# Kernel tuning notes

Hardware: AMD Instinct MI355X
Metric: run time of the kernel (lower is better)

Reference implementation:

```python
import jax, jax.numpy as jnp
import numpy as np

N, E = 100000, 1600000
ENT, OCU, SAI, IJ = 64, 64, 64, 8


def setup_inputs() -> dict:
    key = jax.random.key(0)
    ks = jax.random.split(key, 14)

    def lin(k, fan_in, fan_out):
        s = 1.0 / np.sqrt(fan_in)
        kw, kb = jax.random.split(k)
        w = jax.random.uniform(kw, (fan_in, fan_out), minval=-s, maxval=s, dtype=jnp.float32)
        b = jax.random.uniform(kb, (fan_out,), minval=-s, maxval=s, dtype=jnp.float32)
        return w, b

    we_w1, we_b1 = lin(ks[0], 2 * ENT + 1 + IJ, OCU)
    we_w2, we_b2 = lin(ks[1], OCU, OCU)
    wx_w1, wx_b1 = lin(ks[2], OCU, OCU)
    wx_w2, wx_b2 = lin(ks[3], OCU, 1)
    wh_w1, wh_b1 = lin(ks[4], ENT + OCU, OCU)
    wh_w2, wh_b2 = lin(ks[5], OCU, SAI)
    wv_w1, wv_b1 = lin(ks[6], ENT, OCU)
    wv_w2, wv_b2 = lin(ks[7], OCU, 1)

    return {
        "h": jax.random.normal(ks[8], (N, ENT), dtype=jnp.float32),
        "x": jax.random.normal(ks[9], (N, 3), dtype=jnp.float32),
        "velocidade": jax.random.normal(ks[10], (N, 3), dtype=jnp.float32),
        "atributos_arestas": jax.random.normal(ks[11], (E, IJ), dtype=jnp.float32),
        "we_w1": we_w1, "we_b1": we_b1, "we_w2": we_w2, "we_b2": we_b2,
        "wx_w1": wx_w1, "wx_b1": wx_b1, "wx_w2": wx_w2, "wx_b2": wx_b2,
        "wh_w1": wh_w1, "wh_b1": wh_b1, "wh_w2": wh_w2, "wh_b2": wh_b2,
        "wv_w1": wv_w1, "wv_b1": wv_b1, "wv_w2": wv_w2, "wv_b2": wv_b2,
        "arestas": jax.random.randint(ks[12], (2, E), 0, N, dtype=jnp.int32),
    }


def reference(h, x, velocidade, atributos_arestas,
              we_w1, we_b1, we_w2, we_b2,
              wx_w1, wx_b1, wx_w2, wx_b2,
              wh_w1, wh_b1, wh_w2, wh_b2,
              wv_w1, wv_b1, wv_w2, wv_b2,
              arestas):
    linhas, cols = arestas[0], arestas[1]
    n = h.shape[0]

    # gather endpoint coordinates, radial distance per edge
    diferenca = x[linhas] - x[cols]                            # [E, 3]
    dif_radial = jnp.sum(diferenca * diferenca, axis=1, keepdims=True)  # [E, 1]

    # edge MLP phi_e on [h_i, h_j, ||x_i-x_j||^2, edge_attr]
    atributos = jnp.concatenate([h[linhas], h[cols], dif_radial, atributos_arestas], axis=1)
    m_ij = jnp.tanh(jnp.tanh(atributos @ we_w1 + we_b1) @ we_w2 + we_b2)   # [E, OCU]

    # phi_x: per-edge scalar gate on coordinate differences
    phi_x = jnp.tanh(jnp.tanh(m_ij @ wx_w1 + wx_b1) @ wx_w2 + wx_b2)       # [E, 1]

    # phi_v: per-node scalar gate on velocity
    phi_v = jnp.tanh(h @ wv_w1 + wv_b1) @ wv_w2 + wv_b2                    # [N, 1]

    # segment-mean of (diferenca * phi_x) over source nodes
    trans = diferenca * phi_x                                              # [E, 3]
    agg_sum = jax.ops.segment_sum(trans, linhas, num_segments=n)           # [N, 3]
    cnt = jax.ops.segment_sum(jnp.ones((E, 1), trans.dtype), linhas, num_segments=n)
    agg_mean = agg_sum / jnp.maximum(cnt, 1.0)

    velocidade_nova = velocidade * phi_v + agg_mean
    x_nova = x + velocidade_nova

    # segment-sum of edge messages, node update phi_h
    m_i = jax.ops.segment_sum(m_ij, linhas, num_segments=n)                # [N, OCU]
    h_cat = jnp.concatenate([h, m_i], axis=1)
    h_nova = jnp.tanh(h_cat @ wh_w1 + wh_b1) @ wh_w2 + wh_b2               # [N, SAI]

    return (h_nova, x_nova, velocidade_nova)
```

## Files before the change

### kernel.cpp

```cpp
#include <hip/hip_runtime.h>


typedef unsigned int uint;
typedef unsigned short u16;
typedef __attribute__((ext_vector_type(8))) short short8;
typedef __attribute__((ext_vector_type(4))) float f32x4;

#define UB_LO(u) __uint_as_float((u) << 16)
#define UB_HI(u) __uint_as_float((u) & 0xffff0000u)

__device__ __forceinline__ float fast_tanh(float x) {
    float e = __expf(2.0f * x);
    return 1.0f - 2.0f * __builtin_amdgcn_rcpf(e + 1.0f);
}
__device__ __forceinline__ u16 bf16rne(float f) {
    uint u = __float_as_uint(f);
    return (u16)((u + 0x7fffu + ((u >> 16) & 1u)) >> 16);
}
__device__ __forceinline__ uint packbf(float a, float b) {
    return (uint)bf16rne(a) | ((uint)bf16rne(b) << 16);
}
__device__ __forceinline__ uint packbf_fast(float a, float b) {
    return __builtin_amdgcn_perm(__float_as_uint(b), __float_as_uint(a), 0x07060302u);
}
__device__ __forceinline__ u16 trunc16(float f) {
    return (u16)(__float_as_uint(f) >> 16);
}
__device__ __forceinline__ int swzb(int b) { return b ^ ((b >> 3) & 0x70); }

__global__ void wprep_kernel(const float* __restrict__ we_w1, const float* __restrict__ we_w2,
                             const float* __restrict__ wx_w1, const float* __restrict__ wv_w1,
                             const float* __restrict__ wh_w1, const float* __restrict__ wh_w2,
                             u16* __restrict__ we1t, u16* __restrict__ we2t,
                             u16* __restrict__ wx1t, u16* __restrict__ wv1t,
                             u16* __restrict__ wh1t, u16* __restrict__ wh2t,
                             u16* __restrict__ wert) {
    int t = blockIdx.x * 256 + threadIdx.x;
    if (t < 8192) {
        int j = t >> 7, k = t & 127;
        we1t[t] = bf16rne(we_w1[k * 64 + j]);
        wh1t[t] = bf16rne(wh_w1[k * 64 + j]);
    }
    if (t < 4096) {
        int n = t >> 6, k = t & 63;
        we2t[t] = bf16rne(we_w2[k * 64 + n]);
        wx1t[t] = bf16rne(wx_w1[k * 64 + n]);
        wv1t[t] = bf16rne(wv_w1[k * 64 + n]);
        wh2t[t] = bf16rne(wh_w2[k * 64 + n]);
    }
    if (t < 2048) {
        int n = t >> 5, k = t & 31;
        float v = 0.0f;
        if (k == 0) v = we_w1[128 * 64 + n];
        else if (k <= 8) v = we_w1[(128 + k) * 64 + n];
        wert[t] = bf16rne(v);
    }
}

__global__ __launch_bounds__(256, 4)
void pre_mfma_kernel(const float* __restrict__ h, const float* __restrict__ we_b1,
                     const u16* __restrict__ we1t,
                     u16* __restrict__ HrB, u16* __restrict__ HcB, int N)
{
    __shared__ u16 X1[4096];
    __shared__ u16 X2[4096];
    const int tid = threadIdx.x, lane = tid & 63, wv = tid >> 6;
    const int nb = blockIdx.x * 64;
    const int el = tid >> 2, jg = tid & 3;
    const int fn = lane & 15, fk8 = (lane >> 4) * 8;

    {
        uint pk[8];
        if (nb + el < N) {
            const float4* h4 = (const float4*)(h + (size_t)(nb + el) * 64 + jg * 16);
            #pragma unroll
            for (int q = 0; q < 4; q++) {
                float4 v = h4[q];
                pk[2*q]   = packbf_fast(v.x, v.y);
                pk[2*q+1] = packbf_fast(v.z, v.w);
            }
        } else {
            #pragma unroll
            for (int q = 0; q < 8; q++) pk[q] = 0;
        }
        const int b0 = swzb(el * 128 + jg * 32), b1 = swzb(el * 128 + jg * 32 + 16);
        *(uint4*)(&X1[b0 >> 1]) = make_uint4(pk[0], pk[1], pk[2], pk[3]);
        *(uint4*)(&X1[b1 >> 1]) = make_uint4(pk[4], pk[5], pk[6], pk[7]);
    }
    __syncthreads();

    const int mb = wv * 16;
    short8 a0, a1;
    {
        const int ba = swzb((mb + fn) * 128 + fk8 * 2);
        const int bb = swzb((mb + fn) * 128 + 64 + fk8 * 2);
        a0 = *(const short8*)(&X1[ba >> 1]);
        a1 = *(const short8*)(&X1[bb >> 1]);
    }
    #pragma unroll
    for (int n0 = 0; n0 < 4; n0++) {
        uint4 bw0 = *(const uint4*)(we1t + (n0*16 + fn) * 128 + fk8);
        uint4 bw1 = *(const uint4*)(we1t + (n0*16 + fn) * 128 + 32 + fk8);
        const float bias = we_b1[n0 * 16 + fn];
        f32x4 q = {bias, bias, bias, bias};
        q = __builtin_amdgcn_mfma_f32_16x16x32_bf16(a0, __builtin_bit_cast(short8, bw0), q, 0, 0, 0);
        q = __builtin_amdgcn_mfma_f32_16x16x32_bf16(a1, __builtin_bit_cast(short8, bw1), q, 0, 0, 0);
        #pragma unroll
        for (int r2 = 0; r2 < 4; r2++) {
            const int m = mb + (lane >> 4) * 4 + r2;
            X2[swzb(m * 128 + (n0*16 + fn) * 2) >> 1] = bf16rne(q[r2]);
        }
    }
    __syncthreads();
    if (nb + el < N) {
        const int b0 = swzb(el * 128 + jg * 32), b1 = swzb(el * 128 + jg * 32 + 16);
        uint4 v0 = *(const uint4*)(&X2[b0 >> 1]);
        uint4 v1 = *(const uint4*)(&X2[b1 >> 1]);
        u16* o = HrB + (size_t)(nb + el) * 64 + jg * 16;
        *(uint4*)o = v0; *(uint4*)(o + 8) = v1;
    }
    __syncthreads();
    #pragma unroll
    for (int n0 = 0; n0 < 4; n0++) {
        uint4 bw0 = *(const uint4*)(we1t + (n0*16 + fn) * 128 + 64 + fk8);
        uint4 bw1 = *(const uint4*)(we1t + (n0*16 + fn) * 128 + 96 + fk8);
        f32x4 q = {0.f, 0.f, 0.f, 0.f};
        q = __builtin_amdgcn_mfma_f32_16x16x32_bf16(a0, __builtin_bit_cast(short8, bw0), q, 0, 0, 0);
        q = __builtin_amdgcn_mfma_f32_16x16x32_bf16(a1, __builtin_bit_cast(short8, bw1), q, 0, 0, 0);
        #pragma unroll
        for (int r2 = 0; r2 < 4; r2++) {
            const int m = mb + (lane >> 4) * 4 + r2;
            X2[swzb(m * 128 + (n0*16 + fn) * 2) >> 1] = bf16rne(q[r2]);
        }
    }
    __syncthreads();
    if (nb + el < N) {
        const int b0 = swzb(el * 128 + jg * 32), b1 = swzb(el * 128 + jg * 32 + 16);
        uint4 v0 = *(const uint4*)(&X2[b0 >> 1]);
        uint4 v1 = *(const uint4*)(&X2[b1 >> 1]);
        u16* o = HcB + (size_t)(nb + el) * 64 + jg * 16;
        *(uint4*)o = v0; *(uint4*)(o + 8) = v1;
    }
}

__global__ __launch_bounds__(256, 8)
void edge_mfma_kernel(const float* __restrict__ x, const float* __restrict__ eattr,
                      const int* __restrict__ perm, const int2* __restrict__ rc,
                      const u16* __restrict__ HrB, const u16* __restrict__ HcB,
                      const u16* __restrict__ wert,
                      const u16* __restrict__ we2t, const float* __restrict__ we_b2,
                      const u16* __restrict__ wx1t, const float* __restrict__ wx_b1,
                      const float* __restrict__ wx_w2, const float* __restrict__ wx_b2,
                      float* __restrict__ miF, float* __restrict__ aggF,
                      float* __restrict__ cntF, int E)
{
    __shared__ u16 T[4096];
    __shared__ float dS[64][3];
    __shared__ float pxS[64];
    __shared__ float radS[64];
    __shared__ int rS[64];

    const int tid = threadIdx.x, lane = tid & 63, wv = tid >> 6;
    int bid = blockIdx.x;
    const int nwg = gridDim.x;
    if ((nwg & 7) == 0) bid = (bid & 7) * (nwg >> 3) + (bid >> 3);
    const int sb = bid * 64;
    const int fn = lane & 15, fk8 = (lane >> 4) * 8;
    const int el = tid >> 2, jg = tid & 3;
    const int s = sb + el;
    const int mb = wv * 16;

    {
        int r = -1, c = 0;
        if (s < E) { int2 p2 = rc[s]; r = p2.x; c = p2.y; }
        if (jg == 0) rS[el] = r;
        uint pk[8];
        if (s < E) {
            if (jg == 0) {
                const float d0 = x[(size_t)r*3+0] - x[(size_t)c*3+0];
                const float d1 = x[(size_t)r*3+1] - x[(size_t)c*3+1];
                const float d2 = x[(size_t)r*3+2] - x[(size_t)c*3+2];
                dS[el][0] = d0; dS[el][1] = d1; dS[el][2] = d2;
                radS[el] = d0*d0 + d1*d1 + d2*d2;
            }
            uint4 ra = *(const uint4*)(HrB + (size_t)r * 64 + jg * 16);
            uint4 rb = *(const uint4*)(HrB + (size_t)r * 64 + jg * 16 + 8);
            uint4 ca = *(const uint4*)(HcB + (size_t)c * 64 + jg * 16);
            uint4 cb = *(const uint4*)(HcB + (size_t)c * 64 + jg * 16 + 8);
            uint rw[8] = {ra.x, ra.y, ra.z, ra.w, rb.x, rb.y, rb.z, rb.w};
            uint cw[8] = {ca.x, ca.y, ca.z, ca.w, cb.x, cb.y, cb.z, cb.w};
            #pragma unroll
            for (int q = 0; q < 8; q++) {
                const float lo = UB_LO(rw[q]) + UB_LO(cw[q]);
                const float hi = UB_HI(rw[q]) + UB_HI(cw[q]);
                pk[q] = packbf_fast(lo, hi);
            }
        } else {
            #pragma unroll
            for (int q = 0; q < 8; q++) pk[q] = 0;
        }
        const int b0 = swzb(el * 128 + jg * 32), b1 = swzb(el * 128 + jg * 32 + 16);
        *(uint4*)(&T[b0 >> 1]) = make_uint4(pk[0], pk[1], pk[2], pk[3]);
        *(uint4*)(&T[b1 >> 1]) = make_uint4(pk[4], pk[5], pk[6], pk[7]);
    }
    __syncthreads();

    uint ae[4] = {0, 0, 0, 0};
    {
        const int kc = lane >> 4;
        const int s2 = sb + mb + fn;
        if (kc < 2 && s2 < E) {
            const int e2 = perm[s2];
            const float4* ea4 = (const float4*)(eattr + (size_t)e2 * 8);
            if (kc == 0) {
                float4 u0 = ea4[0], u1 = ea4[1];
                const float rad = radS[mb + fn];
                ae[0] = packbf_fast(rad,  u0.x);
                ae[1] = packbf_fast(u0.y, u0.z);
                ae[2] = packbf_fast(u0.w, u1.x);
                ae[3] = packbf_fast(u1.y, u1.z);
            } else {
                float4 u1 = ea4[1];
                ae[0] = packbf_fast(u1.w, 0.0f);
            }
        }
    }
    const short8 a_e = __builtin_bit_cast(short8, *(uint4*)ae);

    #pragma unroll
    for (int n0 = 0; n0 < 4; n0++) {
        uint4 bw = *(const uint4*)(wert + (n0*16 + fn) * 32 + fk8);
        f32x4 q = {0.f, 0.f, 0.f, 0.f};
        q = __builtin_amdgcn_mfma_f32_16x16x32_bf16(a_e, __builtin_bit_cast(short8, bw), q, 0, 0, 0);
        #pragma unroll
        for (int r2 = 0; r2 < 4; r2++) {
            const int idx = swzb((mb + (lane >> 4) * 4 + r2) * 128 + (n0*16 + fn) * 2) >> 1;
            const float pre = q[r2] + UB_LO((uint)T[idx]);
            T[idx] = trunc16(fast_tanh(pre));
        }
    }

    short8 a0, a1;
    {
        const int ba = swzb((mb + fn) * 128 + fk8 * 2);
        const int bb = swzb((mb + fn) * 128 + 64 + fk8 * 2);
        a0 = *(const short8*)(&T[ba >> 1]);
        a1 = *(const short8*)(&T[bb >> 1]);
    }
    #pragma unroll
    for (int n0 = 0; n0 < 4; n0++) {
        uint4 bw0 = *(const uint4*)(we2t + (n0*16 + fn) * 64 + fk8);
        uint4 bw1 = *(const uint4*)(we2t + (n0*16 + fn) * 64 + 32 + fk8);
        const float bias = we_b2[n0 * 16 + fn];
        f32x4 q = {bias, bias, bias, bias};
        q = __builtin_amdgcn_mfma_f32_16x16x32_bf16(a0, __builtin_bit_cast(short8, bw0), q, 0, 0, 0);
        q = __builtin_amdgcn_mfma_f32_16x16x32_bf16(a1, __builtin_bit_cast(short8, bw1), q, 0, 0, 0);
        #pragma unroll
        for (int r2 = 0; r2 < 4; r2++) {
            const int m = mb + (lane >> 4) * 4 + r2;
            T[swzb(m * 128 + (n0*16 + fn) * 2) >> 1] = bf16rne(fast_tanh(q[r2]));
        }
    }

    short8 c0, c1;
    {
        const int ba = swzb((mb + fn) * 128 + fk8 * 2);
        const int bb = swzb((mb + fn) * 128 + 64 + fk8 * 2);
        c0 = *(const short8*)(&T[ba >> 1]);
        c1 = *(const short8*)(&T[bb >> 1]);
    }
    float pxp[4] = {0.f, 0.f, 0.f, 0.f};
    #pragma unroll
    for (int n0 = 0; n0 < 4; n0++) {
        uint4 bw0 = *(const uint4*)(wx1t + (n0*16 + fn) * 64 + fk8);
        uint4 bw1 = *(const uint4*)(wx1t + (n0*16 + fn) * 64 + 32 + fk8);
        const float bias = wx_b1[n0 * 16 + fn];
        f32x4 q = {bias, bias, bias, bias};
        q = __builtin_amdgcn_mfma_f32_16x16x32_bf16(c0, __builtin_bit_cast(short8, bw0), q, 0, 0, 0);
        q = __builtin_amdgcn_mfma_f32_16x16x32_bf16(c1, __builtin_bit_cast(short8, bw1), q, 0, 0, 0);
        const float wqn = wx_w2[n0 * 16 + fn];
        #pragma unroll
        for (int r2 = 0; r2 < 4; r2++) pxp[r2] += fast_tanh(q[r2]) * wqn;
    }
    #pragma unroll
    for (int off = 1; off < 16; off <<= 1) {
        #pragma unroll
        for (int r2 = 0; r2 < 4; r2++) pxp[r2] += __shfl_xor(pxp[r2], off, 64);
    }
    if (fn == 0) {
        const float bx2 = wx_b2[0];
        #pragma unroll
        for (int r2 = 0; r2 < 4; r2++) {
            const int m = mb + (lane >> 4) * 4 + r2;
            pxS[m] = fast_tanh(pxp[r2] + bx2);
        }
    }
    __syncthreads();

    const int w16 = wv * 16;
    for (int s0 = w16; s0 < w16 + 16; s0++) {
        const int r0 = rS[s0];
        if (r0 < 0) continue;
        if (s0 > 0 && rS[s0 - 1] == r0) continue;
        int s1 = s0 + 1;
        while (s1 < 64 && rS[s1] == r0) s1++;
        float msum = 0.0f, tsum = 0.0f;
        for (int t = s0; t < s1; t++) {
            msum += UB_LO((uint)T[swzb(t * 128 + lane * 2) >> 1]);
            if (lane < 3) tsum += dS[t][lane] * pxS[t];
        }
        atomicAdd(&miF[(size_t)r0 * 64 + lane], msum);
        if (lane < 3) atomicAdd(&aggF[(size_t)r0 * 3 + lane], tsum);
        if (lane == 3) atomicAdd(&cntF[r0], (float)(s1 - s0));
    }
}

__global__ __launch_bounds__(256, 4)
void aggnode_kernel(const float* __restrict__ h, const float* __restrict__ x,
                    const float* __restrict__ vel,
                    const float* __restrict__ miF, const float* __restrict__ aggF,
                    const float* __restrict__ cntF,
                    const u16* __restrict__ wv1t, const float* __restrict__ wv_b1,
                    const float* __restrict__ wv_w2, const float* __restrict__ wv_b2,
                    const u16* __restrict__ wh1t, const float* __restrict__ wh_b1,
                    const u16* __restrict__ wh2t, const float* __restrict__ wh_b2,
                    float* __restrict__ out_h, float* __restrict__ out_x,
                    float* __restrict__ out_v, int N)
{
    __shared__ u16 Xh[4096];
    __shared__ u16 Xm[4096];
    __shared__ float aggM[64][3];
    __shared__ float pvS[64];

    const int tid = threadIdx.x, lane = tid & 63, wv = tid >> 6;
    const int nb = blockIdx.x * 64;
    const int el = tid >> 2, jg = tid & 3;
    const int fn = lane & 15, fk8 = (lane >> 4) * 8;

    {
        uint pk[8];
        if (nb + el < N) {
            const float4* h4 = (const float4*)(h + (size_t)(nb + el) * 64 + jg * 16);
            #pragma unroll
            for (int q = 0; q < 4; q++) {
                float4 v = h4[q];
                pk[2*q]   = packbf_fast(v.x, v.y);
                pk[2*q+1] = packbf_fast(v.z, v.w);
            }
        } else {
            #pragma unroll
            for (int q = 0; q < 8; q++) pk[q] = 0;
        }
        const int b0 = swzb(el * 128 + jg * 32), b1 = swzb(el * 128 + jg * 32 + 16);
        *(uint4*)(&Xh[b0 >> 1]) = make_uint4(pk[0], pk[1], pk[2], pk[3]);
        *(uint4*)(&Xh[b1 >> 1]) = make_uint4(pk[4], pk[5], pk[6], pk[7]);
    }

    for (int t = 0; t < 16; t++) {
        const int ln = wv * 16 + t;
        const int n = nb + ln;
        float val = 0.0f;
        if (n < N) val = miF[(size_t)n * 64 + lane];
        Xm[swzb(ln * 128 + lane * 2) >> 1] = bf16rne(val);
        if (lane < 3 && n < N) {
            const float cf = cntF[n];
            aggM[ln][lane] = aggF[(size_t)n * 3 + lane] / fmaxf(cf, 1.0f);
        }
    }
    __syncthreads();

    const int mb = wv * 16;
    short8 a0, a1, b0, b1;
    {
        const int ba = swzb((mb + fn) * 128 + fk8 * 2);
        const int bb = swzb((mb + fn) * 128 + 64 + fk8 * 2);
        a0 = *(const short8*)(&Xh[ba >> 1]);
        a1 = *(const short8*)(&Xh[bb >> 1]);
        b0 = *(const short8*)(&Xm[ba >> 1]);
        b1 = *(const short8*)(&Xm[bb >> 1]);
    }

    float pvp[4] = {0.f, 0.f, 0.f, 0.f};
    #pragma unroll
    for (int n0 = 0; n0 < 4; n0++) {
        uint4 bw0 = *(const uint4*)(wv1t + (n0*16 + fn) * 64 + fk8);
        uint4 bw1 = *(const uint4*)(wv1t + (n0*16 + fn) * 64 + 32 + fk8);
        const float bias = wv_b1[n0 * 16 + fn];
        f32x4 q = {bias, bias, bias, bias};
        q = __builtin_amdgcn_mfma_f32_16x16x32_bf16(a0, __builtin_bit_cast(short8, bw0), q, 0, 0, 0);
        q = __builtin_amdgcn_mfma_f32_16x16x32_bf16(a1, __builtin_bit_cast(short8, bw1), q, 0, 0, 0);
        const float wqn = wv_w2[n0 * 16 + fn];
        #pragma unroll
        for (int r2 = 0; r2 < 4; r2++) pvp[r2] += fast_tanh(q[r2]) * wqn;
    }
    #pragma unroll
    for (int off = 1; off < 16; off <<= 1) {
        #pragma unroll
        for (int r2 = 0; r2 < 4; r2++) pvp[r2] += __shfl_xor(pvp[r2], off, 64);
    }
    if (fn == 0) {
        const float bv2 = wv_b2[0];
        #pragma unroll
        for (int r2 = 0; r2 < 4; r2++) pvS[mb + (lane >> 4) * 4 + r2] = pvp[r2] + bv2;
    }
    __syncthreads();

    #pragma unroll
    for (int n0 = 0; n0 < 4; n0++) {
        const u16* base = wh1t + (n0*16 + fn) * 128;
        uint4 bw0 = *(const uint4*)(base + fk8);
        uint4 bw1 = *(const uint4*)(base + 32 + fk8);
        uint4 bw2 = *(const uint4*)(base + 64 + fk8);
        uint4 bw3 = *(const uint4*)(base + 96 + fk8);
        const float bias = wh_b1[n0 * 16 + fn];
        f32x4 q = {bias, bias, bias, bias};
        q = __builtin_amdgcn_mfma_f32_16x16x32_bf16(a0, __builtin_bit_cast(short8, bw0), q, 0, 0, 0);
        q = __builtin_amdgcn_mfma_f32_16x16x32_bf16(a1, __builtin_bit_cast(short8, bw1), q, 0, 0, 0);
        q = __builtin_amdgcn_mfma_f32_16x16x32_bf16(b0, __builtin_bit_cast(short8, bw2), q, 0, 0, 0);
        q = __builtin_amdgcn_mfma_f32_16x16x32_bf16(b1, __builtin_bit_cast(short8, bw3), q, 0, 0, 0);
        #pragma unroll
        for (int r2 = 0; r2 < 4; r2++) {
            const int m = mb + (lane >> 4) * 4 + r2;
            Xm[swzb(m * 128 + (n0*16 + fn) * 2) >> 1] = bf16rne(fast_tanh(q[r2]));
        }
    }
    __syncthreads();

    short8 c0, c1;
    {
        const int ba = swzb((mb + fn) * 128 + fk8 * 2);
        const int bb = swzb((mb + fn) * 128 + 64 + fk8 * 2);
        c0 = *(const short8*)(&Xm[ba >> 1]);
        c1 = *(const short8*)(&Xm[bb >> 1]);
    }
    #pragma unroll
    for (int n0 = 0; n0 < 4; n0++) {
        uint4 bw0 = *(const uint4*)(wh2t + (n0*16 + fn) * 64 + fk8);
        uint4 bw1 = *(const uint4*)(wh2t + (n0*16 + fn) * 64 + 32 + fk8);
        const float bias = wh_b2[n0 * 16 + fn];
        f32x4 q = {bias, bias, bias, bias};
        q = __builtin_amdgcn_mfma_f32_16x16x32_bf16(c0, __builtin_bit_cast(short8, bw0), q, 0, 0, 0);
        q = __builtin_amdgcn_mfma_f32_16x16x32_bf16(c1, __builtin_bit_cast(short8, bw1), q, 0, 0, 0);
        #pragma unroll
        for (int r2 = 0; r2 < 4; r2++) {
            const int m = mb + (lane >> 4) * 4 + r2;
            if (nb + m < N) out_h[(size_t)(nb + m) * 64 + n0 * 16 + fn] = q[r2];
        }
    }

    if (tid < 64 && nb + tid < N) {
        const int n = nb + tid;
        const float pv = pvS[tid];
        #pragma unroll
        for (int d = 0; d < 3; d++) {
            const float am = aggM[tid][d];
            const float vn = vel[(size_t)n * 3 + d] * pv + am;
            out_v[(size_t)n * 3 + d] = vn;
            out_x[(size_t)n * 3 + d] = x[(size_t)n * 3 + d] + vn;
        }
    }
}

__global__ void hist_kernel(const int* __restrict__ rows, int* __restrict__ hist, int E) {
    int e = blockIdx.x * blockDim.x + threadIdx.x;
    if (e < E) atomicAdd(&hist[rows[e]], 1);
}

__global__ __launch_bounds__(256)
void scan1_kernel(const int* __restrict__ hist, int* __restrict__ bsum, int N) {
    const int t = threadIdx.x, b = blockIdx.x;
    const int base = b * 1024 + t * 4;
    int s = 0;
    #pragma unroll
    for (int q = 0; q < 4; q++) s += (base + q < N) ? hist[base + q] : 0;
    #pragma unroll
    for (int off = 1; off < 64; off <<= 1) s += __shfl_xor(s, off, 64);
    __shared__ int ws[4];
    if ((t & 63) == 0) ws[t >> 6] = s;
    __syncthreads();
    if (t == 0) bsum[b] = ws[0] + ws[1] + ws[2] + ws[3];
}

__global__ __launch_bounds__(256)
void scan2_kernel(int* __restrict__ bsum, int nb) {
    __shared__ int buf[1024];
    const int t = threadIdx.x;
    for (int i = t; i < nb; i += 256) buf[i] = bsum[i];
    __syncthreads();
    if (t == 0) {
        int run = 0;
        for (int i = 0; i < nb; i++) { int v = buf[i]; buf[i] = run; run += v; }
    }
    __syncthreads();
    for (int i = t; i < nb; i += 256) bsum[i] = buf[i];
}

__global__ __launch_bounds__(256)
void scan3_kernel(const int* __restrict__ hist, const int* __restrict__ bbase,
                  int* __restrict__ offs, int* __restrict__ cursor, int N) {
    const int t = threadIdx.x, b = blockIdx.x;
    const int base = b * 1024 + t * 4;
    int v[4];
    #pragma unroll
    for (int q = 0; q < 4; q++) v[q] = (base + q < N) ? hist[base + q] : 0;
    const int s = v[0] + v[1] + v[2] + v[3];
    const int lane = t & 63, wid = t >> 6;
    int inc = s;
    #pragma unroll
    for (int off = 1; off < 64; off <<= 1) {
        int u = __shfl_up(inc, off, 64);
        if (lane >= off) inc += u;
    }
    __shared__ int wtot[4];
    if (lane == 63) wtot[wid] = inc;
    __syncthreads();
    int wbase = 0;
    #pragma unroll
    for (int wq = 0; wq < 3; wq++) if (wq < wid) wbase += wtot[wq];
    int run = bbase[b] + wbase + (inc - s);
    #pragma unroll
    for (int q = 0; q < 4; q++) {
        const int i = base + q;
        if (i < N) { cursor[i] = run; run += v[q]; offs[i + 1] = run; }
    }
    if (b == 0 && t == 0) offs[0] = 0;
}

__global__ void scatter_kernel(const int* __restrict__ rows, const int* __restrict__ cols,
                               int* __restrict__ cursor,
                               int* __restrict__ perm, int2* __restrict__ rc, int E) {
    int e = blockIdx.x * blockDim.x + threadIdx.x;
    if (e < E) {
        int r = rows[e];
        int p = atomicAdd(&cursor[r], 1);
        perm[p] = e;
        rc[p] = make_int2(r, cols[e]);
    }
}

template<int BLK>
__global__ __launch_bounds__(BLK)
void edge_atomic_kernel(const float* __restrict__ h, const float* __restrict__ x,
                 const float* __restrict__ eattr,
                 const int* __restrict__ rows, const int* __restrict__ cols,
                 const float* __restrict__ we_w1, const float* __restrict__ we_b1,
                 const float* __restrict__ we_w2, const float* __restrict__ we_b2,
                 const float* __restrict__ wx_w1, const float* __restrict__ wx_b1,
                 const float* __restrict__ wx_w2, const float* __restrict__ wx_b2,
                 float* __restrict__ agg, float* __restrict__ cnt, float* __restrict__ mi,
                 int E)
{
    __shared__ float act[64][BLK];
    const int tid = threadIdx.x;
    const int e = blockIdx.x * BLK + tid;
    if (e >= E) return;

    const int r = rows[e];
    const int c = cols[e];
    const float d0 = x[(size_t)r*3+0] - x[(size_t)c*3+0];
    const float d1 = x[(size_t)r*3+1] - x[(size_t)c*3+1];
    const float d2 = x[(size_t)r*3+2] - x[(size_t)c*3+2];
    const float rad = d0*d0 + d1*d1 + d2*d2;

    float A[64];
    #pragma unroll
    for (int j = 0; j < 64; j++) A[j] = we_b1[j];
    const float* hr = h + (size_t)r * 64;
    const float* hc = h + (size_t)c * 64;
    #pragma unroll 4
    for (int k = 0; k < 64; k++) {
        const float a0 = hr[k];
        const float a1 = hc[k];
        const float* w0 = we_w1 + k * 64;
        const float* w1 = we_w1 + (64 + k) * 64;
        #pragma unroll
        for (int j = 0; j < 64; j++) A[j] += a0 * w0[j] + a1 * w1[j];
    }
    {
        const float* w = we_w1 + 128 * 64;
        #pragma unroll
        for (int j = 0; j < 64; j++) A[j] += rad * w[j];
    }
    const float* ea = eattr + (size_t)e * 8;
    #pragma unroll
    for (int k = 0; k < 8; k++) {
        const float a = ea[k];
        const float* w = we_w1 + (129 + k) * 64;
        #pragma unroll
        for (int j = 0; j < 64; j++) A[j] += a * w[j];
    }
    #pragma unroll
    for (int j = 0; j < 64; j++) act[j][tid] = fast_tanh(A[j]);

    float B[64];
    #pragma unroll
    for (int j = 0; j < 64; j++) B[j] = we_b2[j];
    #pragma unroll 4
    for (int k = 0; k < 64; k++) {
        const float a = act[k][tid];
        const float* w = we_w2 + k * 64;
        #pragma unroll
        for (int j = 0; j < 64; j++) B[j] += a * w[j];
    }
    #pragma unroll
    for (int j = 0; j < 64; j++) act[j][tid] = fast_tanh(B[j]);

    #pragma unroll
    for (int j = 0; j < 64; j++) A[j] = wx_b1[j];
    #pragma unroll 4
    for (int k = 0; k < 64; k++) {
        const float a = act[k][tid];
        const float* w = wx_w1 + k * 64;
        #pragma unroll
        for (int j = 0; j < 64; j++) A[j] += a * w[j];
    }
    float px = wx_b2[0];
    #pragma unroll
    for (int j = 0; j < 64; j++) px += fast_tanh(A[j]) * wx_w2[j];
    px = fast_tanh(px);

    atomicAdd(&agg[(size_t)r*3+0], d0 * px);
    atomicAdd(&agg[(size_t)r*3+1], d1 * px);
    atomicAdd(&agg[(size_t)r*3+2], d2 * px);
    atomicAdd(&cnt[r], 1.0f);
    float* mir = mi + (size_t)r * 64;
    #pragma unroll
    for (int j = 0; j < 64; j++) atomicAdd(&mir[j], act[j][tid]);
}

template<int BLK>
__global__ __launch_bounds__(BLK, 2)
void node_fb_kernel(const float* __restrict__ h, const float* __restrict__ x,
                 const float* __restrict__ vel,
                 const float* __restrict__ wh_w1, const float* __restrict__ wh_b1,
                 const float* __restrict__ wh_w2, const float* __restrict__ wh_b2,
                 const float* __restrict__ wv_w1, const float* __restrict__ wv_b1,
                 const float* __restrict__ wv_w2, const float* __restrict__ wv_b2,
                 const float* __restrict__ agg, const float* __restrict__ cnt,
                 const float* __restrict__ mi,
                 float* __restrict__ out_h, float* __restrict__ out_x, float* __restrict__ out_v,
                 int N)
{
    const int n = blockIdx.x * BLK + threadIdx.x;
    if (n >= N) return;

    const float* hn = h + (size_t)n * 64;
    const float* mn = mi + (size_t)n * 64;

    float A[64];
    #pragma unroll
    for (int j = 0; j < 64; j++) A[j] = wv_b1[j];
    #pragma unroll
    for (int k = 0; k < 64; k++) {
        const float a = hn[k];
        const float* w = wv_w1 + k * 64;
        #pragma unroll
        for (int j = 0; j < 64; j++) A[j] += a * w[j];
    }
    float pv = wv_b2[0];
    #pragma unroll
    for (int j = 0; j < 64; j++) pv += fast_tanh(A[j]) * wv_w2[j];

    #pragma unroll
    for (int j = 0; j < 64; j++) A[j] = wh_b1[j];
    #pragma unroll
    for (int k = 0; k < 64; k++) {
        const float a0 = hn[k];
        const float a1 = mn[k];
        const float* w0 = wh_w1 + k * 64;
        const float* w1 = wh_w1 + (64 + k) * 64;
        #pragma unroll
        for (int j = 0; j < 64; j++) A[j] += a0 * w0[j] + a1 * w1[j];
    }
    #pragma unroll
    for (int j = 0; j < 64; j++) A[j] = fast_tanh(A[j]);

    float B[64];
    #pragma unroll
    for (int j = 0; j < 64; j++) B[j] = wh_b2[j];
    #pragma unroll
    for (int k = 0; k < 64; k++) {
        const float a = A[k];
        const float* w = wh_w2 + k * 64;
        #pragma unroll
        for (int j = 0; j < 64; j++) B[j] += a * w[j];
    }
    float* oh = out_h + (size_t)n * 64;
    #pragma unroll
    for (int j = 0; j < 64; j++) oh[j] = B[j];

    const float inv = 1.0f / fmaxf(cnt[n], 1.0f);
    #pragma unroll
    for (int d = 0; d < 3; d++) {
        const float am = agg[(size_t)n*3 + d] * inv;
        const float vn = vel[(size_t)n*3 + d] * pv + am;
        out_v[(size_t)n*3 + d] = vn;
        out_x[(size_t)n*3 + d] = x[(size_t)n*3 + d] + vn;
    }
}

extern "C" void kernel_launch(void* const* d_in, const int* in_sizes, int n_in,
                              void* d_out, int out_size, void* d_ws, size_t ws_size,
                              hipStream_t stream) {
    const float* h      = (const float*)d_in[0];
    const float* x      = (const float*)d_in[1];
    const float* vel    = (const float*)d_in[2];
    const float* eattr  = (const float*)d_in[3];
    const float* we_w1  = (const float*)d_in[4];
    const float* we_b1  = (const float*)d_in[5];
    const float* we_w2  = (const float*)d_in[6];
    const float* we_b2  = (const float*)d_in[7];
    const float* wx_w1  = (const float*)d_in[8];
    const float* wx_b1  = (const float*)d_in[9];
    const float* wx_w2  = (const float*)d_in[10];
    const float* wx_b2  = (const float*)d_in[11];
    const float* wh_w1  = (const float*)d_in[12];
    const float* wh_b1  = (const float*)d_in[13];
    const float* wh_w2  = (const float*)d_in[14];
    const float* wh_b2  = (const float*)d_in[15];
    const float* wv_w1  = (const float*)d_in[16];
    const float* wv_b1  = (const float*)d_in[17];
    const float* wv_w2  = (const float*)d_in[18];
    const float* wv_b2  = (const float*)d_in[19];
    const int*   ar     = (const int*)d_in[20];

    const int N = in_sizes[0] / 64;
    const int E = in_sizes[20] / 2;
    const int* rows = ar;
    const int* cols = ar + E;

    float* out_h = (float*)d_out;
    float* out_x = out_h + (size_t)N * 64;
    float* out_v = out_x + (size_t)N * 3;

    u16* HrB = (u16*)d_out;
    u16* HcB = HrB + (size_t)N * 64;

    const int nbScan = (N + 1023) / 1024;

    char* p = (char*)d_ws;
    float* miF  = (float*)p; p += (size_t)N * 64 * sizeof(float);
    float* aggF = (float*)p; p += (size_t)N * 3 * sizeof(float);
    float* cntF = (float*)p; p += (size_t)N * sizeof(float);
    int*  hist  = (int*)p;   p += (size_t)N * sizeof(int);
    const size_t zero_bytes = (size_t)(p - (char*)d_ws);
    int*  offs  = (int*)p;   p += (size_t)(N + 1) * sizeof(int);
    int*  cursor= (int*)p;   p += (size_t)N * sizeof(int);
    int*  bsum  = (int*)p;   p += (size_t)(nbScan > 0 ? nbScan : 1) * sizeof(int);
    int*  perm  = (int*)p;   p += (size_t)E * sizeof(int);
    p = (char*)(((uintptr_t)p + 7) & ~(uintptr_t)7);
    int2* rc    = (int2*)p;  p += (size_t)E * sizeof(int2);
    p = (char*)(((uintptr_t)p + 63) & ~(uintptr_t)63);
    u16*  we1t = (u16*)p;   p += 64 * 128 * sizeof(u16);
    u16*  we2t = (u16*)p;   p += 64 * 64 * sizeof(u16);
    u16*  wx1t = (u16*)p;   p += 64 * 64 * sizeof(u16);
    u16*  wv1t = (u16*)p;   p += 64 * 64 * sizeof(u16);
    u16*  wh1t = (u16*)p;   p += 64 * 128 * sizeof(u16);
    u16*  wh2t = (u16*)p;   p += 64 * 64 * sizeof(u16);
    u16*  wert = (u16*)p;   p += 64 * 32 * sizeof(u16);
    const size_t needed = (size_t)(p - (char*)d_ws);

    if (ws_size >= needed && nbScan <= 1024) {
        hipMemsetAsync(d_ws, 0, zero_bytes, stream);
        hist_kernel<<<(E + 255) / 256, 256, 0, stream>>>(rows, hist, E);
        scan1_kernel<<<nbScan, 256, 0, stream>>>(hist, bsum, N);
        scan2_kernel<<<1, 256, 0, stream>>>(bsum, nbScan);
        scan3_kernel<<<nbScan, 256, 0, stream>>>(hist, bsum, offs, cursor, N);
        scatter_kernel<<<(E + 255) / 256, 256, 0, stream>>>(rows, cols, cursor, perm, rc, E);

        wprep_kernel<<<32, 256, 0, stream>>>(we_w1, we_w2, wx_w1, wv_w1, wh_w1, wh_w2,
                                             we1t, we2t, wx1t, wv1t, wh1t, wh2t, wert);
        pre_mfma_kernel<<<(N + 63) / 64, 256, 0, stream>>>(h, we_b1, we1t, HrB, HcB, N);

        edge_mfma_kernel<<<(E + 63) / 64, 256, 0, stream>>>(
            x, eattr, perm, rc, HrB, HcB,
            wert, we2t, we_b2, wx1t, wx_b1, wx_w2, wx_b2,
            miF, aggF, cntF, E);

        aggnode_kernel<<<(N + 63) / 64, 256, 0, stream>>>(
            h, x, vel, miF, aggF, cntF,
            wv1t, wv_b1, wv_w2, wv_b2,
            wh1t, wh_b1, wh2t, wh_b2,
            out_h, out_x, out_v, N);
    } else {
        float* agg2 = (float*)d_ws;
        float* cnt2 = agg2 + (size_t)N * 3;
        float* mi2  = cnt2 + N;
        hipMemsetAsync(d_ws, 0, (size_t)N * 68 * sizeof(float), stream);

        edge_atomic_kernel<128><<<(E + 127) / 128, 128, 0, stream>>>(
            h, x, eattr, rows, cols,
            we_w1, we_b1, we_w2, we_b2,
            wx_w1, wx_b1, wx_w2, wx_b2,
            agg2, cnt2, mi2, E);

        node_fb_kernel<128><<<(N + 127) / 128, 128, 0, stream>>>(
            h, x, vel,
            wh_w1, wh_b1, wh_w2, wh_b2,
            wv_w1, wv_b1, wv_w2, wv_b2,
            agg2, cnt2, mi2, out_h, out_x, out_v, N);
    }
}
```

Measured before the change: 550.4 us.

## Pack sorted edge records, fuse weight prep into histogram, ballot-based segment reduce

Merges the weight-conversion kernel into the histogram kernel to save one launch. Replaces the separate perm and row/col arrays with a single 16-byte record per sorted edge, so the edge kernel reads the original edge id from shared memory instead of doing a second dependent global load. The per-wave segment search for runs of equal source rows now uses a wave ballot and bit scans instead of serial shared-memory scans. The records are wider than before (16 bytes versus 12), which adds write and read traffic in the scatter and edge kernels.

Measured after the change: 555.8 us, median of 2. No clear change (+1.0%).

```diff
diff --git a/kernel.cpp b/kernel.cpp
--- a/kernel.cpp
+++ b/kernel.cpp
@@ -28,32 +28,39 @@
 }
 __device__ __forceinline__ int swzb(int b) { return b ^ ((b >> 3) & 0x70); }
 
-__global__ void wprep_kernel(const float* __restrict__ we_w1, const float* __restrict__ we_w2,
-                             const float* __restrict__ wx_w1, const float* __restrict__ wv_w1,
-                             const float* __restrict__ wh_w1, const float* __restrict__ wh_w2,
-                             u16* __restrict__ we1t, u16* __restrict__ we2t,
-                             u16* __restrict__ wx1t, u16* __restrict__ wv1t,
-                             u16* __restrict__ wh1t, u16* __restrict__ wh2t,
-                             u16* __restrict__ wert) {
-    int t = blockIdx.x * 256 + threadIdx.x;
-    if (t < 8192) {
-        int j = t >> 7, k = t & 127;
-        we1t[t] = bf16rne(we_w1[k * 64 + j]);
-        wh1t[t] = bf16rne(wh_w1[k * 64 + j]);
-    }
-    if (t < 4096) {
-        int n = t >> 6, k = t & 63;
-        we2t[t] = bf16rne(we_w2[k * 64 + n]);
-        wx1t[t] = bf16rne(wx_w1[k * 64 + n]);
-        wv1t[t] = bf16rne(wv_w1[k * 64 + n]);
-        wh2t[t] = bf16rne(wh_w2[k * 64 + n]);
-    }
-    if (t < 2048) {
-        int n = t >> 5, k = t & 31;
-        float v = 0.0f;
-        if (k == 0) v = we_w1[128 * 64 + n];
-        else if (k <= 8) v = we_w1[(128 + k) * 64 + n];
-        wert[t] = bf16rne(v);
+__global__ void wprep_hist_kernel(const float* __restrict__ we_w1, const float* __restrict__ we_w2,
+                                  const float* __restrict__ wx_w1, const float* __restrict__ wv_w1,
+                                  const float* __restrict__ wh_w1, const float* __restrict__ wh_w2,
+                                  u16* __restrict__ we1t, u16* __restrict__ we2t,
+                                  u16* __restrict__ wx1t, u16* __restrict__ wv1t,
+                                  u16* __restrict__ wh1t, u16* __restrict__ wh2t,
+                                  u16* __restrict__ wert,
+                                  const int* __restrict__ rows, int* __restrict__ hist, int E) {
+    const int b = blockIdx.x;
+    if (b < 32) {
+        int t = b * 256 + threadIdx.x;
+        if (t < 8192) {
+            int j = t >> 7, k = t & 127;
+            we1t[t] = bf16rne(we_w1[k * 64 + j]);
+            wh1t[t] = bf16rne(wh_w1[k * 64 + j]);
+        }
+        if (t < 4096) {
+            int n = t >> 6, k = t & 63;
+            we2t[t] = bf16rne(we_w2[k * 64 + n]);
+            wx1t[t] = bf16rne(wx_w1[k * 64 + n]);
+            wv1t[t] = bf16rne(wv_w1[k * 64 + n]);
+            wh2t[t] = bf16rne(wh_w2[k * 64 + n]);
+        }
+        if (t < 2048) {
+            int n = t >> 5, k = t & 31;
+            float v = 0.0f;
+            if (k == 0) v = we_w1[128 * 64 + n];
+            else if (k <= 8) v = we_w1[(128 + k) * 64 + n];
+            wert[t] = bf16rne(v);
+        }
+    } else {
+        int e = (b - 32) * 256 + threadIdx.x;
+        if (e < E) atomicAdd(&hist[rows[e]], 1);
     }
 }
 
@@ -145,7 +152,7 @@
 
 __global__ __launch_bounds__(256, 8)
 void edge_mfma_kernel(const float* __restrict__ x, const float* __restrict__ eattr,
-                      const int* __restrict__ perm, const int2* __restrict__ rc,
+                      const uint4* __restrict__ rec4,
                       const u16* __restrict__ HrB, const u16* __restrict__ HcB,
                       const u16* __restrict__ wert,
                       const u16* __restrict__ we2t, const float* __restrict__ we_b2,
@@ -159,6 +166,7 @@
     __shared__ float pxS[64];
     __shared__ float radS[64];
     __shared__ int rS[64];
+    __shared__ int eS[64];
 
     const int tid = threadIdx.x, lane = tid & 63, wv = tid >> 6;
     int bid = blockIdx.x;
@@ -172,7 +180,8 @@
 
     {
         int r = -1, c = 0;
-        if (s < E) { int2 p2 = rc[s]; r = p2.x; c = p2.y; }
+        if (s < E) { uint4 p4 = rec4[s]; r = (int)p4.x; c = (int)p4.y;
+                     if (jg == 0) eS[el] = (int)p4.z; }
         if (jg == 0) rS[el] = r;
         uint pk[8];
         if (s < E) {
@@ -210,7 +219,7 @@
         const int kc = lane >> 4;
         const int s2 = sb + mb + fn;
         if (kc < 2 && s2 < E) {
-            const int e2 = perm[s2];
+            const int e2 = eS[mb + fn];
             const float4* ea4 = (const float4*)(eattr + (size_t)e2 * 8);
             if (kc == 0) {
                 float4 u0 = ea4[0], u1 = ea4[1];
@@ -297,21 +306,27 @@
     }
     __syncthreads();
 
-    const int w16 = wv * 16;
-    for (int s0 = w16; s0 < w16 + 16; s0++) {
-        const int r0 = rS[s0];
-        if (r0 < 0) continue;
-        if (s0 > 0 && rS[s0 - 1] == r0) continue;
-        int s1 = s0 + 1;
-        while (s1 < 64 && rS[s1] == r0) s1++;
-        float msum = 0.0f, tsum = 0.0f;
-        for (int t = s0; t < s1; t++) {
-            msum += UB_LO((uint)T[swzb(t * 128 + lane * 2) >> 1]);
-            if (lane < 3) tsum += dS[t][lane] * pxS[t];
-        }
-        atomicAdd(&miF[(size_t)r0 * 64 + lane], msum);
-        if (lane < 3) atomicAdd(&aggF[(size_t)r0 * 3 + lane], tsum);
-        if (lane == 3) atomicAdd(&cntF[r0], (float)(s1 - s0));
+    {
+        const int rl = rS[lane];
+        const int rp = (lane > 0) ? rS[lane - 1] : -2;
+        const unsigned long long startm = __ballot(lane == 0 || rl != rp);
+        unsigned long long m = startm & (0xFFFFull << (wv * 16));
+        while (m) {
+            const int s0 = (int)__builtin_ctzll(m);
+            m &= m - 1;
+            const int r0 = rS[s0];
+            if (r0 < 0) continue;
+            const unsigned long long rest = (startm >> s0) >> 1;
+            const int s1 = rest ? s0 + 1 + (int)__builtin_ctzll(rest) : 64;
+            float msum = 0.0f, tsum = 0.0f;
+            for (int t = s0; t < s1; t++) {
+                msum += UB_LO((uint)T[swzb(t * 128 + lane * 2) >> 1]);
+                if (lane < 3) tsum += dS[t][lane] * pxS[t];
+            }
+            atomicAdd(&miF[(size_t)r0 * 64 + lane], msum);
+            if (lane < 3) atomicAdd(&aggF[(size_t)r0 * 3 + lane], tsum);
+            if (lane == 3) atomicAdd(&cntF[r0], (float)(s1 - s0));
+        }
     }
 }
 
@@ -461,11 +476,6 @@
     }
 }
 
-__global__ void hist_kernel(const int* __restrict__ rows, int* __restrict__ hist, int E) {
-    int e = blockIdx.x * blockDim.x + threadIdx.x;
-    if (e < E) atomicAdd(&hist[rows[e]], 1);
-}
-
 __global__ __launch_bounds__(256)
 void scan1_kernel(const int* __restrict__ hist, int* __restrict__ bsum, int N) {
     const int t = threadIdx.x, b = blockIdx.x;
@@ -527,14 +537,12 @@
 }
 
 __global__ void scatter_kernel(const int* __restrict__ rows, const int* __restrict__ cols,
-                               int* __restrict__ cursor,
-                               int* __restrict__ perm, int2* __restrict__ rc, int E) {
+                               int* __restrict__ cursor, uint4* __restrict__ rec4, int E) {
     int e = blockIdx.x * blockDim.x + threadIdx.x;
     if (e < E) {
         int r = rows[e];
         int p = atomicAdd(&cursor[r], 1);
-        perm[p] = e;
-        rc[p] = make_int2(r, cols[e]);
+        rec4[p] = make_uint4((uint)r, (uint)cols[e], (uint)e, 0u);
     }
 }
 
@@ -747,9 +755,8 @@
     int*  offs  = (int*)p;   p += (size_t)(N + 1) * sizeof(int);
     int*  cursor= (int*)p;   p += (size_t)N * sizeof(int);
     int*  bsum  = (int*)p;   p += (size_t)(nbScan > 0 ? nbScan : 1) * sizeof(int);
-    int*  perm  = (int*)p;   p += (size_t)E * sizeof(int);
-    p = (char*)(((uintptr_t)p + 7) & ~(uintptr_t)7);
-    int2* rc    = (int2*)p;  p += (size_t)E * sizeof(int2);
+    p = (char*)(((uintptr_t)p + 15) & ~(uintptr_t)15);
+    uint4* rec4 = (uint4*)p; p += (size_t)E * sizeof(uint4);
     p = (char*)(((uintptr_t)p + 63) & ~(uintptr_t)63);
     u16*  we1t = (u16*)p;   p += 64 * 128 * sizeof(u16);
     u16*  we2t = (u16*)p;   p += 64 * 64 * sizeof(u16);
@@ -762,18 +769,18 @@
 
     if (ws_size >= needed && nbScan <= 1024) {
         hipMemsetAsync(d_ws, 0, zero_bytes, stream);
-        hist_kernel<<<(E + 255) / 256, 256, 0, stream>>>(rows, hist, E);
+        wprep_hist_kernel<<<32 + (E + 255) / 256, 256, 0, stream>>>(
+            we_w1, we_w2, wx_w1, wv_w1, wh_w1, wh_w2,
+            we1t, we2t, wx1t, wv1t, wh1t, wh2t, wert, rows, hist, E);
         scan1_kernel<<<nbScan, 256, 0, stream>>>(hist, bsum, N);
         scan2_kernel<<<1, 256, 0, stream>>>(bsum, nbScan);
         scan3_kernel<<<nbScan, 256, 0, stream>>>(hist, bsum, offs, cursor, N);
-        scatter_kernel<<<(E + 255) / 256, 256, 0, stream>>>(rows, cols, cursor, perm, rc, E);
-
-        wprep_kernel<<<32, 256, 0, stream>>>(we_w1, we_w2, wx_w1, wv_w1, wh_w1, wh_w2,
-                                             we1t, we2t, wx1t, wv1t, wh1t, wh2t, wert);
+        scatter_kernel<<<(E + 255) / 256, 256, 0, stream>>>(rows, cols, cursor, rec4, E);
+
         pre_mfma_kernel<<<(N + 63) / 64, 256, 0, stream>>>(h, we_b1, we1t, HrB, HcB, N);
 
         edge_mfma_kernel<<<(E + 63) / 64, 256, 0, stream>>>(
-            x, eattr, perm, rc, HrB, HcB,
+            x, eattr, rec4, HrB, HcB,
             wert, we2t, we_b2, wx1t, wx_b1, wx_w2, wx_b2,
             miF, aggF, cntF, E);
 
```
